# Performance work log

Measured on AMD Instinct MI355X. Metric: run time of the kernel, lower is better.

## Reference

```python
import jax, jax.numpy as jnp
import numpy as np

B, S, E, H = 4, 2048, 1024, 16
D = E // H  # head dim = 64


def setup_inputs() -> dict:
    key = jax.random.key(0)
    ks = jax.random.split(key, 9)
    s_in = 1.0 / np.sqrt(E)
    return {
        "x": jax.random.normal(ks[0], (B, S, E), dtype=jnp.float32),
        # stacked per-head projection weights, acting as x @ W + b
        "Wq": jax.random.normal(ks[1], (H, E, D), dtype=jnp.float32) * s_in,
        "bq": jax.random.normal(ks[2], (H, D), dtype=jnp.float32) * 0.01,
        "Wk": jax.random.normal(ks[3], (H, E, D), dtype=jnp.float32) * s_in,
        "bk": jax.random.normal(ks[4], (H, D), dtype=jnp.float32) * 0.01,
        "Wv": jax.random.normal(ks[5], (H, E, D), dtype=jnp.float32) * s_in,
        "bv": jax.random.normal(ks[6], (H, D), dtype=jnp.float32) * 0.01,
        "Wo": jax.random.normal(ks[7], (E, E), dtype=jnp.float32) * s_in,
        "bo": jax.random.normal(ks[8], (E,), dtype=jnp.float32) * 0.01,
    }


def reference(x, Wq, bq, Wk, bk, Wv, bv, Wo, bo):
    # Batched per-head projections (equivalent to the per-head nn.Linear loop)
    q = jnp.einsum("bse,hed->bhsd", x, Wq) + bq[None, :, None, :]
    k = jnp.einsum("bse,hed->bhsd", x, Wk) + bk[None, :, None, :]
    v = jnp.einsum("bse,hed->bhsd", x, Wv) + bv[None, :, None, :]
    scale = 1.0 / jnp.sqrt(jnp.asarray(D, dtype=x.dtype))
    scores = jnp.einsum("bhsd,bhtd->bhst", q, k) * scale  # [B,H,S,S]
    attn = jax.nn.softmax(scores, axis=-1)
    ctx = jnp.einsum("bhst,bhtd->bhsd", attn, v)  # [B,H,S,D]
    # torch.cat over heads along last dim -> [B,S,H*D]=[B,S,E]
    ctx = jnp.transpose(ctx, (0, 2, 1, 3)).reshape(x.shape[0], x.shape[1], E)
    return ctx @ Wo + bo
```

## Files before the change

kernel.cpp:

```cpp
#include <hip/hip_runtime.h>
#include <math.h>

#define B_ 4
#define S_ 2048
#define E_ 1024
#define H_ 16
#define D_ 64
#define BH_ (B_ * H_)

#define SCALE_LOG2E 0.18033688011112042f

typedef short short8 __attribute__((ext_vector_type(8)));
typedef float f32x4 __attribute__((ext_vector_type(4)));
typedef float f32x16 __attribute__((ext_vector_type(16)));

static __device__ __forceinline__ unsigned short f2bf(float f) {
    unsigned int u = __float_as_uint(f);
    unsigned int r = (u + 0x7fffu + ((u >> 16) & 1u)) >> 16;
    return (unsigned short)r;
}

static __device__ __forceinline__ unsigned int pack_bf16_trunc(float hi, float lo) {
    return __builtin_amdgcn_perm(__float_as_uint(hi), __float_as_uint(lo), 0x07060302u);
}

static __device__ __forceinline__ void gl_lds16(const unsigned short* g, unsigned short* l) {
    __builtin_amdgcn_global_load_lds(
        (const __attribute__((address_space(1))) unsigned int*)g,
        (__attribute__((address_space(3))) unsigned int*)l, 16, 0, 0);
}


__global__ __launch_bounds__(256) void xcvt_kernel(
    const float* __restrict__ x, unsigned short* __restrict__ Xb)
{
    size_t i = ((size_t)blockIdx.x * 256 + threadIdx.x) * 8;
    float4 a = *(const float4*)&x[i];
    float4 b = *(const float4*)&x[i + 4];
    ushort4 u0, u1;
    u0.x = f2bf(a.x); u0.y = f2bf(a.y); u0.z = f2bf(a.z); u0.w = f2bf(a.w);
    u1.x = f2bf(b.x); u1.y = f2bf(b.y); u1.z = f2bf(b.z); u1.w = f2bf(b.w);
    *(ushort4*)&Xb[i]     = u0;
    *(ushort4*)&Xb[i + 4] = u1;
}

__global__ __launch_bounds__(256) void wtrans_qkv_kernel(
    const float* __restrict__ Wq, const float* __restrict__ Wk,
    const float* __restrict__ Wv, unsigned short* __restrict__ Wt)
{
    __shared__ float t[32][33];
    const int tx = threadIdx.x & 31, ty = threadIdx.x >> 5;
    const int r0 = blockIdx.x * 32, c0 = blockIdx.y * 32;
    const int z = blockIdx.z, mtx = z >> 4, h = z & 15;
    const float* s = (mtx == 0 ? Wq : (mtx == 1 ? Wk : Wv)) + (size_t)h * E_ * D_;
    const float scale = (mtx == 0) ? SCALE_LOG2E : 1.0f;
    unsigned short* d = Wt + (size_t)mtx * E_ * E_ + (size_t)h * D_ * E_;
#pragma unroll
    for (int i = 0; i < 4; ++i)
        t[ty + i * 8][tx] = s[(size_t)(r0 + ty + i * 8) * D_ + c0 + tx];
    __syncthreads();
#pragma unroll
    for (int i = 0; i < 4; ++i)
        d[(size_t)(c0 + ty + i * 8) * E_ + r0 + tx] = f2bf(t[tx][ty + i * 8] * scale);
}

__global__ __launch_bounds__(256) void wtrans_kernel(
    const float* __restrict__ src, unsigned short* __restrict__ dst, int R, int C)
{
    __shared__ float t[32][33];
    const int tx = threadIdx.x & 31, ty = threadIdx.x >> 5;
    const int r0 = blockIdx.x * 32, c0 = blockIdx.y * 32;
#pragma unroll
    for (int i = 0; i < 4; ++i)
        t[ty + i * 8][tx] = src[(size_t)(r0 + ty + i * 8) * C + c0 + tx];
    __syncthreads();
#pragma unroll
    for (int i = 0; i < 4; ++i)
        dst[(size_t)(c0 + ty + i * 8) * R + r0 + tx] = f2bf(t[tx][ty + i * 8]);
}

__global__ __launch_bounds__(256) void qkv_gemm_kernel(
    const unsigned short* __restrict__ Xb, const unsigned short* __restrict__ Wt,
    const float* __restrict__ bq, const float* __restrict__ bk,
    const float* __restrict__ bv,
    unsigned short* __restrict__ Qh, unsigned short* __restrict__ Kh,
    unsigned short* __restrict__ Vth)
{
    __shared__ unsigned short As[2][128 * 64];
    __shared__ unsigned short Bs[2][128 * 64];
    const int tid = threadIdx.x;
    const int lane = tid & 63, wid = tid >> 6;
    const int quad = lane >> 4, lc = lane & 15;
    const int wm = wid >> 1, wn = wid & 1;
    const int m0 = blockIdx.y * 128, n0 = blockIdx.x * 128;
    const int l8 = lane >> 3;
    const int sch = ((lane & 7) ^ l8) * 8;

    f32x4 acc[4][4];
#pragma unroll
    for (int mt = 0; mt < 4; ++mt)
#pragma unroll
        for (int nt = 0; nt < 4; ++nt)
            acc[mt][nt] = (f32x4){0.f, 0.f, 0.f, 0.f};

#pragma unroll
    for (int i = 0; i < 4; ++i) {
        int rw = wid * 32 + i * 8;
        gl_lds16(&Xb[(size_t)(m0 + rw + l8) * E_ + sch], &As[0][rw * 64]);
        gl_lds16(&Wt[(size_t)(n0 + rw + l8) * E_ + sch], &Bs[0][rw * 64]);
    }
    __syncthreads();

    for (int k0 = 0; k0 < E_; k0 += 64) {
        const int cur = (k0 >> 6) & 1;
        if (k0 + 64 < E_) {
#pragma unroll
            for (int i = 0; i < 4; ++i) {
                int rw = wid * 32 + i * 8;
                gl_lds16(&Xb[(size_t)(m0 + rw + l8) * E_ + k0 + 64 + sch], &As[cur ^ 1][rw * 64]);
                gl_lds16(&Wt[(size_t)(n0 + rw + l8) * E_ + k0 + 64 + sch], &Bs[cur ^ 1][rw * 64]);
            }
        }
#pragma unroll
        for (int kc = 0; kc < 2; ++kc) {
            short8 a[4], bfr[4];
#pragma unroll
            for (int mt = 0; mt < 4; ++mt)
                a[mt] = *(const short8*)&As[cur][(wm * 64 + mt * 16 + lc) * 64 +
                                                (((kc * 4 + quad) ^ (lc & 7)) << 3)];
#pragma unroll
            for (int nt = 0; nt < 4; ++nt)
                bfr[nt] = *(const short8*)&Bs[cur][(wn * 64 + nt * 16 + lc) * 64 +
                                                  (((kc * 4 + quad) ^ (lc & 7)) << 3)];
#pragma unroll
            for (int mt = 0; mt < 4; ++mt)
#pragma unroll
                for (int nt = 0; nt < 4; ++nt)
                    acc[mt][nt] = __builtin_amdgcn_mfma_f32_16x16x32_bf16(
                        a[mt], bfr[nt], acc[mt][nt], 0, 0, 0);
        }
        __syncthreads();
    }

    const int nb = n0 + wn * 64;
    const int mtx = nb >> 10;
    const int h = (nb >> 6) & 15;
    const int sg0 = m0 + wm * 64;
    const int bb_ = sg0 >> 11;
    if (mtx < 2) {
        const float bsc = (mtx == 0) ? SCALE_LOG2E : 1.0f;
        const float* bias = (mtx == 0 ? bq : bk) + h * D_;
        unsigned short* Out = (mtx == 0) ? Qh : Kh;
#pragma unroll
        for (int nt = 0; nt < 4; ++nt) {
            int d = nt * 16 + lc;
            float bb = bias[d] * bsc;
#pragma unroll
            for (int mt = 0; mt < 4; ++mt)
#pragma unroll
                for (int r = 0; r < 4; ++r) {
                    int ss = (sg0 + mt * 16 + quad * 4 + r) & (S_ - 1);
                    Out[((size_t)(bb_ * H_ + h) * S_ + ss) * D_ + d] =
                        f2bf(acc[mt][nt][r] + bb);
                }
        }
    } else {
        const float* bias = bv + h * D_;
#pragma unroll
        for (int nt = 0; nt < 4; ++nt) {
            int d = nt * 16 + lc;
            float bb = bias[d];
#pragma unroll
            for (int mt = 0; mt < 4; ++mt) {
                int ss0 = (sg0 + mt * 16 + quad * 4) & (S_ - 1);
                ushort4 u;
                u.x = f2bf(acc[mt][nt][0] + bb);
                u.y = f2bf(acc[mt][nt][1] + bb);
                u.z = f2bf(acc[mt][nt][2] + bb);
                u.w = f2bf(acc[mt][nt][3] + bb);
                *(ushort4*)&Vth[(((size_t)bb_ * H_ + h) * D_ + d) * S_ + ss0] = u;
            }
        }
    }
}

__global__ __launch_bounds__(256, 4) void attn_kernel(
    const unsigned short* __restrict__ Qh, const unsigned short* __restrict__ Kh,
    const unsigned short* __restrict__ Vth, unsigned short* __restrict__ Ch)
{
    __shared__ unsigned short ks[2][64 * 64];
    __shared__ unsigned short vt[2][64 * 64];
    const int tid = threadIdx.x;
    const int lane = tid & 63, wid = tid >> 6;
    const int l31 = lane & 31, hi = lane >> 5;
    const int bh = blockIdx.x, b = bh >> 4, h = bh & 15;
    const int q0 = blockIdx.y * 128;
    const size_t base  = (size_t)bh * S_ * D_;
    const size_t vbase = (size_t)bh * D_ * S_;
    const int l8 = lane >> 3;
    const int sch = ((lane & 7) ^ l8) * 8;

    unsigned short* qstage = &ks[0][0];
#pragma unroll
    for (int i = 0; i < 4; ++i) {
        int rw = wid * 32 + i * 8;
        gl_lds16(&Qh[base + (size_t)(q0 + rw + l8) * D_ + sch], &qstage[rw * 64]);
    }
    __syncthreads();
    short8 qf[4];
    {
        const int qrow = wid * 32 + l31;
#pragma unroll
        for (int kc = 0; kc < 4; ++kc)
            qf[kc] = *(const short8*)&qstage[qrow * 64 +
                                             (((kc * 2 + hi) ^ (qrow & 7)) << 3)];
    }
    __syncthreads();

#pragma unroll
    for (int i = 0; i < 2; ++i) {
        int rw = wid * 16 + i * 8;
        gl_lds16(&Kh[base + (size_t)(rw + l8) * D_ + sch], &ks[0][rw * 64]);
        gl_lds16(&Vth[vbase + (size_t)(rw + l8) * S_ + sch], &vt[0][rw * 64]);
    }
    __syncthreads();

    short8 ones;
#pragma unroll
    for (int i = 0; i < 8; ++i) ones[i] = (short)0x3F80;

    f32x16 ctx[2], lacc;
#pragma unroll
    for (int i = 0; i < 16; ++i) { ctx[0][i] = 0.f; ctx[1][i] = 0.f; lacc[i] = 0.f; }

    for (int kt = 0; kt < S_; kt += 64) {
        const int cur = (kt >> 6) & 1;
        if (kt + 64 < S_) {
#pragma unroll
            for (int i = 0; i < 2; ++i) {
                int rw = wid * 16 + i * 8;
                gl_lds16(&Kh[base + (size_t)(kt + 64 + rw + l8) * D_ + sch],
                         &ks[cur ^ 1][rw * 64]);
                gl_lds16(&Vth[vbase + (size_t)(rw + l8) * S_ + kt + 64 + sch],
                         &vt[cur ^ 1][rw * 64]);
            }
        }

#pragma unroll
        for (int kb = 0; kb < 2; ++kb) {
            f32x16 st;
#pragma unroll
            for (int i = 0; i < 16; ++i) st[i] = 0.f;
            const int krow = kb * 32 + l31;
#pragma unroll
            for (int kc = 0; kc < 4; ++kc) {
                short8 kf = *(const short8*)&ks[cur][krow * 64 +
                                                    (((kc * 2 + hi) ^ (krow & 7)) << 3)];
                st = __builtin_amdgcn_mfma_f32_32x32x16_bf16(kf, qf[kc], st, 0, 0, 0);
            }

#pragma unroll
            for (int ks16 = 0; ks16 < 2; ++ks16) {
                float e0 = __builtin_amdgcn_exp2f(st[8 * ks16 + 0]);
                float e1 = __builtin_amdgcn_exp2f(st[8 * ks16 + 1]);
                float e2 = __builtin_amdgcn_exp2f(st[8 * ks16 + 2]);
                float e3 = __builtin_amdgcn_exp2f(st[8 * ks16 + 3]);
                float e4 = __builtin_amdgcn_exp2f(st[8 * ks16 + 4]);
                float e5 = __builtin_amdgcn_exp2f(st[8 * ks16 + 5]);
                float e6 = __builtin_amdgcn_exp2f(st[8 * ks16 + 6]);
                float e7 = __builtin_amdgcn_exp2f(st[8 * ks16 + 7]);
                unsigned int w0 = pack_bf16_trunc(e1, e0);
                unsigned int w1 = pack_bf16_trunc(e3, e2);
                unsigned int w2 = pack_bf16_trunc(e5, e4);
                unsigned int w3 = pack_bf16_trunc(e7, e6);
                asm("v_permlane32_swap_b32 %0, %1" : "+v"(w0), "+v"(w2));
                asm("v_permlane32_swap_b32 %0, %1" : "+v"(w1), "+v"(w3));
                union { unsigned int u[4]; short8 s; } pu;
                pu.u[0] = w0; pu.u[1] = w1; pu.u[2] = w2; pu.u[3] = w3;
                const short8 pf = pu.s;

                lacc = __builtin_amdgcn_mfma_f32_32x32x16_bf16(pf, ones, lacc, 0, 0, 0);
#pragma unroll
                for (int dsub = 0; dsub < 2; ++dsub) {
                    const int vrow = dsub * 32 + l31;
                    short8 vf = *(const short8*)&vt[cur][vrow * 64 +
                        (((kb * 4 + ks16 * 2 + hi) ^ (vrow & 7)) << 3)];
                    ctx[dsub] = __builtin_amdgcn_mfma_f32_32x32x16_bf16(
                        pf, vf, ctx[dsub], 0, 0, 0);
                }
            }
        }
        __syncthreads();
    }

#pragma unroll
    for (int r = 0; r < 16; ++r) {
        float inv = 1.f / lacc[r];
        int q = q0 + wid * 32 + (r & 3) + ((r >> 2) << 3) + hi * 4;
        size_t rowbase = ((size_t)b * S_ + q) * E_ + h * D_;
        Ch[rowbase + l31]      = f2bf(ctx[0][r] * inv);
        Ch[rowbase + 32 + l31] = f2bf(ctx[1][r] * inv);
    }
}

__global__ __launch_bounds__(256) void out_proj_kernel(
    const unsigned short* __restrict__ Ch, const unsigned short* __restrict__ Wot,
    const float* __restrict__ bo, float* __restrict__ out)
{
    __shared__ unsigned short As[2][128 * 64];
    __shared__ unsigned short Bs[2][128 * 64];
    const int tid = threadIdx.x;
    const int lane = tid & 63, wid = tid >> 6;
    const int quad = lane >> 4, lc = lane & 15;
    const int wm = wid >> 1, wn = wid & 1;
    const int m0 = blockIdx.y * 128, n0 = blockIdx.x * 128;
    const int l8 = lane >> 3;
    const int sch = ((lane & 7) ^ l8) * 8;

    f32x4 acc[4][4];
#pragma unroll
    for (int mt = 0; mt < 4; ++mt)
#pragma unroll
        for (int nt = 0; nt < 4; ++nt)
            acc[mt][nt] = (f32x4){0.f, 0.f, 0.f, 0.f};

#pragma unroll
    for (int i = 0; i < 4; ++i) {
        int rw = wid * 32 + i * 8;
        gl_lds16(&Ch[(size_t)(m0 + rw + l8) * E_ + sch], &As[0][rw * 64]);
        gl_lds16(&Wot[(size_t)(n0 + rw + l8) * E_ + sch], &Bs[0][rw * 64]);
    }
    __syncthreads();

    for (int k0 = 0; k0 < E_; k0 += 64) {
        const int cur = (k0 >> 6) & 1;
        if (k0 + 64 < E_) {
#pragma unroll
            for (int i = 0; i < 4; ++i) {
                int rw = wid * 32 + i * 8;
                gl_lds16(&Ch[(size_t)(m0 + rw + l8) * E_ + k0 + 64 + sch], &As[cur ^ 1][rw * 64]);
                gl_lds16(&Wot[(size_t)(n0 + rw + l8) * E_ + k0 + 64 + sch], &Bs[cur ^ 1][rw * 64]);
            }
        }
#pragma unroll
        for (int kc = 0; kc < 2; ++kc) {
            short8 a[4], bfr[4];
#pragma unroll
            for (int mt = 0; mt < 4; ++mt)
                a[mt] = *(const short8*)&As[cur][(wm * 64 + mt * 16 + lc) * 64 +
                                                (((kc * 4 + quad) ^ (lc & 7)) << 3)];
#pragma unroll
            for (int nt = 0; nt < 4; ++nt)
                bfr[nt] = *(const short8*)&Bs[cur][(wn * 64 + nt * 16 + lc) * 64 +
                                                  (((kc * 4 + quad) ^ (lc & 7)) << 3)];
#pragma unroll
            for (int mt = 0; mt < 4; ++mt)
#pragma unroll
                for (int nt = 0; nt < 4; ++nt)
                    acc[mt][nt] = __builtin_amdgcn_mfma_f32_16x16x32_bf16(
                        a[mt], bfr[nt], acc[mt][nt], 0, 0, 0);
        }
        __syncthreads();
    }

#pragma unroll
    for (int mt = 0; mt < 4; ++mt)
#pragma unroll
        for (int nt = 0; nt < 4; ++nt) {
            int n = n0 + wn * 64 + nt * 16 + lc;
            float bb = bo[n];
#pragma unroll
            for (int r = 0; r < 4; ++r) {
                int row = m0 + wm * 64 + mt * 16 + quad * 4 + r;
                out[(size_t)row * E_ + n] = acc[mt][nt][r] + bb;
            }
        }
}

extern "C" void kernel_launch(void* const* d_in, const int* in_sizes, int n_in,
                              void* d_out, int out_size, void* d_ws, size_t ws_size,
                              hipStream_t stream)
{
    const float* x  = (const float*)d_in[0];
    const float* Wq = (const float*)d_in[1];
    const float* bq = (const float*)d_in[2];
    const float* Wk = (const float*)d_in[3];
    const float* bk = (const float*)d_in[4];
    const float* Wv = (const float*)d_in[5];
    const float* bv = (const float*)d_in[6];
    const float* Wo = (const float*)d_in[7];
    const float* bo = (const float*)d_in[8];
    (void)in_sizes; (void)n_in; (void)out_size; (void)ws_size;

    const size_t N = (size_t)BH_ * S_ * D_;
    unsigned short* Wt  = (unsigned short*)d_ws;
    unsigned short* Wot = Wt + (size_t)3072 * 1024;
    unsigned short* Xb  = Wot + (size_t)1024 * 1024;
    unsigned short* Qh  = Xb + N;
    unsigned short* Kh  = Qh + N;
    unsigned short* Vth = Kh + N;
    unsigned short* Ch  = Vth + N;

    xcvt_kernel<<<dim3(4096), 256, 0, stream>>>(x, Xb);
    wtrans_qkv_kernel<<<dim3(32, 2, 48), 256, 0, stream>>>(Wq, Wk, Wv, Wt);
    wtrans_kernel<<<dim3(32, 32, 1), 256, 0, stream>>>(Wo, Wot, E_, E_);

    qkv_gemm_kernel<<<dim3(24, 64), 256, 0, stream>>>(Xb, Wt, bq, bk, bv, Qh, Kh, Vth);
    attn_kernel<<<dim3(64, 16), 256, 0, stream>>>(Qh, Kh, Vth, Ch);
    out_proj_kernel<<<dim3(8, 64), 256, 0, stream>>>(Ch, Wot, bo, (float*)d_out);
}
```

Measured before the change: 275.2 us.

## Store Q/K/V in MFMA-fragment-tiled layout and raise wave priority around MFMAs

The QKV projection epilogue now writes Q, K and V^T into a tiled layout where each 512-element chunk matches one MFMA operand fragment. The attention kernel can then load each chunk with lane-contiguous 16-byte global-to-LDS copies and read fragments without XOR swizzle arithmetic. Each chunk is stored in lane order, so contiguous LDS reads should avoid bank conflicts. The change also wraps the MFMA sections in s_setprio to favour matrix-issuing waves. The projection epilogue's scattered per-element stores for Q/K may coalesce differently than before.

```diff
diff --git a/kernel.cpp b/kernel.cpp
--- a/kernel.cpp
+++ b/kernel.cpp
@@ -147,38 +147,45 @@
     const int h = (nb >> 6) & 15;
     const int sg0 = m0 + wm * 64;
     const int bb_ = sg0 >> 11;
+    const int bhv = bb_ * H_ + h;
     if (mtx < 2) {
         const float bsc = (mtx == 0) ? SCALE_LOG2E : 1.0f;
         const float* bias = (mtx == 0 ? bq : bk) + h * D_;
         unsigned short* Out = (mtx == 0) ? Qh : Kh;
+        const size_t obase = (size_t)bhv * (S_ / 32) * 2048;
 #pragma unroll
         for (int nt = 0; nt < 4; ++nt) {
             int d = nt * 16 + lc;
+            int hi_ = (lc >> 3) & 1, j = lc & 7;
             float bb = bias[d] * bsc;
 #pragma unroll
             for (int mt = 0; mt < 4; ++mt)
 #pragma unroll
                 for (int r = 0; r < 4; ++r) {
                     int ss = (sg0 + mt * 16 + quad * 4 + r) & (S_ - 1);
-                    Out[((size_t)(bb_ * H_ + h) * S_ + ss) * D_ + d] =
-                        f2bf(acc[mt][nt][r] + bb);
+                    Out[obase + ((size_t)(ss >> 5) * 4 + nt) * 512 +
+                        ((ss & 31) * 2 + hi_) * 8 + j] = f2bf(acc[mt][nt][r] + bb);
                 }
         }
     } else {
         const float* bias = bv + h * D_;
+        const size_t obase = (size_t)bhv * (S_ / 64) * 4096;
+        const int t64 = (sg0 & (S_ - 1)) >> 6;
+        const int hi_ = quad >> 1, j0 = (quad & 1) * 4;
 #pragma unroll
         for (int nt = 0; nt < 4; ++nt) {
             int d = nt * 16 + lc;
+            int dsub = d >> 5, l31d = d & 31;
             float bb = bias[d];
 #pragma unroll
             for (int mt = 0; mt < 4; ++mt) {
-                int ss0 = (sg0 + mt * 16 + quad * 4) & (S_ - 1);
                 ushort4 u;
                 u.x = f2bf(acc[mt][nt][0] + bb);
                 u.y = f2bf(acc[mt][nt][1] + bb);
                 u.z = f2bf(acc[mt][nt][2] + bb);
                 u.w = f2bf(acc[mt][nt][3] + bb);
-                *(ushort4*)&Vth[(((size_t)bb_ * H_ + h) * D_ + d) * S_ + ss0] = u;
+                *(ushort4*)&Vth[obase + ((size_t)t64 * 8 + mt * 2 + dsub) * 512 +
+                                (l31d * 2 + hi_) * 8 + j0] = u;
             }
         }
     }
@@ -188,40 +195,39 @@
     const unsigned short* __restrict__ Qh, const unsigned short* __restrict__ Kh,
     const unsigned short* __restrict__ Vth, unsigned short* __restrict__ Ch)
 {
-    __shared__ unsigned short ks[2][64 * 64];
-    __shared__ unsigned short vt[2][64 * 64];
+    __shared__ unsigned short ks[2][8 * 512];
+    __shared__ unsigned short vt[2][8 * 512];
     const int tid = threadIdx.x;
     const int lane = tid & 63, wid = tid >> 6;
     const int l31 = lane & 31, hi = lane >> 5;
     const int bh = blockIdx.x, b = bh >> 4, h = bh & 15;
     const int q0 = blockIdx.y * 128;
-    const size_t base  = (size_t)bh * S_ * D_;
-    const size_t vbase = (size_t)bh * D_ * S_;
-    const int l8 = lane >> 3;
-    const int sch = ((lane & 7) ^ l8) * 8;
+    const size_t qkbase = (size_t)bh * (S_ / 32) * 2048;
+    const size_t vbase  = (size_t)bh * (S_ / 64) * 4096;
+    const int rdoff = (l31 * 2 + hi) * 8;
+    const int ldoff = lane * 8;
 
     unsigned short* qstage = &ks[0][0];
-#pragma unroll
-    for (int i = 0; i < 4; ++i) {
-        int rw = wid * 32 + i * 8;
-        gl_lds16(&Qh[base + (size_t)(q0 + rw + l8) * D_ + sch], &qstage[rw * 64]);
+    {
+        const int t32 = (q0 >> 5) + wid;
+#pragma unroll
+        for (int kc = 0; kc < 4; ++kc)
+            gl_lds16(&Qh[qkbase + ((size_t)t32 * 4 + kc) * 512 + ldoff],
+                     &qstage[(wid * 4 + kc) * 512]);
     }
     __syncthreads();
     short8 qf[4];
-    {
-        const int qrow = wid * 32 + l31;
-#pragma unroll
-        for (int kc = 0; kc < 4; ++kc)
-            qf[kc] = *(const short8*)&qstage[qrow * 64 +
-                                             (((kc * 2 + hi) ^ (qrow & 7)) << 3)];
-    }
+#pragma unroll
+    for (int kc = 0; kc < 4; ++kc)
+        qf[kc] = *(const short8*)&qstage[(wid * 4 + kc) * 512 + rdoff];
     __syncthreads();
 
 #pragma unroll
     for (int i = 0; i < 2; ++i) {
-        int rw = wid * 16 + i * 8;
-        gl_lds16(&Kh[base + (size_t)(rw + l8) * D_ + sch], &ks[0][rw * 64]);
-        gl_lds16(&Vth[vbase + (size_t)(rw + l8) * S_ + sch], &vt[0][rw * 64]);
+        int sk = wid * 2 + i;
+        int kb = sk >> 2, kc = sk & 3;
+        gl_lds16(&Kh[qkbase + ((size_t)kb * 4 + kc) * 512 + ldoff], &ks[0][sk * 512]);
+        gl_lds16(&Vth[vbase + (size_t)sk * 512 + ldoff], &vt[0][sk * 512]);
     }
     __syncthreads();
 
@@ -236,13 +242,15 @@
     for (int kt = 0; kt < S_; kt += 64) {
         const int cur = (kt >> 6) & 1;
         if (kt + 64 < S_) {
+            const int ktn = kt + 64;
 #pragma unroll
             for (int i = 0; i < 2; ++i) {
-                int rw = wid * 16 + i * 8;
-                gl_lds16(&Kh[base + (size_t)(kt + 64 + rw + l8) * D_ + sch],
-                         &ks[cur ^ 1][rw * 64]);
-                gl_lds16(&Vth[vbase + (size_t)(rw + l8) * S_ + kt + 64 + sch],
-                         &vt[cur ^ 1][rw * 64]);
+                int sk = wid * 2 + i;
+                int kb = sk >> 2, kc = sk & 3;
+                gl_lds16(&Kh[qkbase + ((size_t)((ktn >> 5) + kb) * 4 + kc) * 512 + ldoff],
+                         &ks[cur ^ 1][sk * 512]);
+                gl_lds16(&Vth[vbase + ((size_t)(ktn >> 6) * 8 + sk) * 512 + ldoff],
+                         &vt[cur ^ 1][sk * 512]);
             }
         }
 
@@ -251,13 +259,13 @@
             f32x16 st;
 #pragma unroll
             for (int i = 0; i < 16; ++i) st[i] = 0.f;
-            const int krow = kb * 32 + l31;
+            __builtin_amdgcn_s_setprio(1);
 #pragma unroll
             for (int kc = 0; kc < 4; ++kc) {
-                short8 kf = *(const short8*)&ks[cur][krow * 64 +
-                                                    (((kc * 2 + hi) ^ (krow & 7)) << 3)];
+                short8 kf = *(const short8*)&ks[cur][(kb * 4 + kc) * 512 + rdoff];
                 st = __builtin_amdgcn_mfma_f32_32x32x16_bf16(kf, qf[kc], st, 0, 0, 0);
             }
+            __builtin_amdgcn_s_setprio(0);
 
 #pragma unroll
             for (int ks16 = 0; ks16 < 2; ++ks16) {
@@ -279,15 +287,15 @@
                 pu.u[0] = w0; pu.u[1] = w1; pu.u[2] = w2; pu.u[3] = w3;
                 const short8 pf = pu.s;
 
+                __builtin_amdgcn_s_setprio(1);
                 lacc = __builtin_amdgcn_mfma_f32_32x32x16_bf16(pf, ones, lacc, 0, 0, 0);
 #pragma unroll
                 for (int dsub = 0; dsub < 2; ++dsub) {
-                    const int vrow = dsub * 32 + l31;
-                    short8 vf = *(const short8*)&vt[cur][vrow * 64 +
-                        (((kb * 4 + ks16 * 2 + hi) ^ (vrow & 7)) << 3)];
+                    short8 vf = *(const short8*)&vt[cur][((kb * 2 + ks16) * 2 + dsub) * 512 + rdoff];
                     ctx[dsub] = __builtin_amdgcn_mfma_f32_32x32x16_bf16(
                         pf, vf, ctx[dsub], 0, 0, 0);
                 }
+                __builtin_amdgcn_s_setprio(0);
             }
         }
         __syncthreads();
```

After: 279.5 us. Within noise of the previous version (+1.6%).
